# Kernel tuning notes

Measured on AMD Instinct MI355X. Metric: run time of the kernel, lower is better.

## Reference

```python
import jax, jax.numpy as jnp
import numpy as np

HIDDEN = 2048
NHEADS = 16
NKV = 4
HEAD_DIM = 128
B, T = 2, 2048


def setup_inputs() -> dict:
    key = jax.random.key(0)
    ks = jax.random.split(key, 7)
    x = jax.random.normal(ks[0], (B, T, HIDDEN), dtype=jnp.float32)
    # rope tables [T, head_dim//2]
    inv_freq = 1.0 / (10000.0 ** (jnp.arange(0, HEAD_DIM // 2, dtype=jnp.float32) / (HEAD_DIM // 2)))
    pos = jnp.arange(T, dtype=jnp.float32)
    ang = pos[:, None] * inv_freq[None, :]
    cos, sin = jnp.cos(ang), jnp.sin(ang)
    s = 0.02
    wq = jax.random.normal(ks[1], (HIDDEN, NHEADS * HEAD_DIM), dtype=jnp.float32) * s
    wk = jax.random.normal(ks[2], (HIDDEN, NKV * HEAD_DIM), dtype=jnp.float32) * s
    wv = jax.random.normal(ks[3], (HIDDEN, NKV * HEAD_DIM), dtype=jnp.float32) * s
    wo = jax.random.normal(ks[4], (NHEADS * HEAD_DIM, HIDDEN), dtype=jnp.float32) * s
    return {"x": x, "cos": cos, "sin": sin, "wq": wq, "wk": wk, "wv": wv, "wo": wo}


def _apply_rope(x, cos, sin):
    # x: [B, H, T, D]; cos/sin: [T, D//2]
    hd = x.shape[-1]
    x1, x2 = x[..., : hd // 2], x[..., hd // 2 :]
    c = cos[None, None, : x.shape[2], :]
    s = sin[None, None, : x.shape[2], :]
    return jnp.concatenate([x1 * c - x2 * s, x2 * c + x1 * s], axis=-1)


def reference(x, cos, sin, wq, wk, wv, wo):
    Bb, Tt, _ = x.shape
    q = (x @ wq).reshape(Bb, Tt, NHEADS, HEAD_DIM).transpose(0, 2, 1, 3)  # [B,H,T,D]
    k = (x @ wk).reshape(Bb, Tt, NKV, HEAD_DIM).transpose(0, 2, 1, 3)    # [B,Hk,T,D]
    v = (x @ wv).reshape(Bb, Tt, NKV, HEAD_DIM).transpose(0, 2, 1, 3)
    q = _apply_rope(q, cos, sin)
    k = _apply_rope(k, cos, sin)
    groups = NHEADS // NKV
    k = jnp.repeat(k, groups, axis=1)  # [B,H,T,D]
    v = jnp.repeat(v, groups, axis=1)
    scale = 1.0 / jnp.sqrt(jnp.asarray(HEAD_DIM, dtype=x.dtype))
    scores = jnp.einsum("bhqd,bhkd->bhqk", q, k) * scale
    causal = jnp.tril(jnp.ones((Tt, Tt), dtype=bool))
    scores = jnp.where(causal[None, None, :, :], scores, jnp.asarray(-jnp.inf, dtype=scores.dtype))
    attn = jax.nn.softmax(scores, axis=-1)
    out = jnp.einsum("bhqk,bhkd->bhqd", attn, v)
    out = out.transpose(0, 2, 1, 3).reshape(Bb, Tt, NHEADS * HEAD_DIM)
    return out @ wo
```

## Files before the change

### kernel.cpp

```cpp
#include <hip/hip_runtime.h>

#define HIDDEN 2048
#define NHEADS 16
#define NKV 4
#define HEAD_DIM 128
#define BB 2
#define TT 2048
#define MROWS (BB * TT)
#define NQKV (NHEADS * HEAD_DIM + 2 * NKV * HEAD_DIM)

typedef __attribute__((ext_vector_type(8))) short short8;
typedef __attribute__((ext_vector_type(4))) float f32x4;

#if __has_builtin(__builtin_amdgcn_exp2f)
#define EXP2F __builtin_amdgcn_exp2f
#else
#define EXP2F exp2f
#endif

__device__ __forceinline__ unsigned short f2bf(float f) {
    unsigned int u = __float_as_uint(f);
    unsigned int r = u + 0x7fffu + ((u >> 16) & 1u);
    return (unsigned short)(r >> 16);
}
__device__ __forceinline__ float b2f(unsigned short h) {
    return __uint_as_float(((unsigned int)h) << 16);
}

__device__ __forceinline__ void store_out(float* p, float v) { *p = v; }
__device__ __forceinline__ void store_out(unsigned short* p, float v) { *p = f2bf(v); }

__device__ __forceinline__ void load_lds_16(const void* g, void* l) {
    __builtin_amdgcn_global_load_lds((const __attribute__((address_space(1))) unsigned int*)g,
                                     (__attribute__((address_space(3))) unsigned int*)l,
                                     16, 0, 0);
}

__global__ void cast_x_kernel(const float* __restrict__ x, unsigned short* __restrict__ xb) {
    int i = blockIdx.x * 256 + threadIdx.x;
    float4 v = ((const float4*)x)[i];
    ushort4 o;
    o.x = f2bf(v.x); o.y = f2bf(v.y); o.z = f2bf(v.z); o.w = f2bf(v.w);
    ((ushort4*)xb)[i] = o;
}

__global__ void pack_wqkvT_kernel(const float* __restrict__ wq, const float* __restrict__ wk,
                                  const float* __restrict__ wv, unsigned short* __restrict__ out) {
    __shared__ float tile[32][33];
    int n0 = blockIdx.x * 32, k0 = blockIdx.y * 32;
    int tx = threadIdx.x, ty = threadIdx.y;
#pragma unroll
    for (int i = 0; i < 32; i += 8) {
        int k = k0 + ty + i;
        int n = n0 + tx;
        float v;
        if (n < 2048)      v = wq[(size_t)k * 2048 + n];
        else if (n < 2560) v = wk[(size_t)k * 512 + (n - 2048)];
        else               v = wv[(size_t)k * 512 + (n - 2560)];
        tile[ty + i][tx] = v;
    }
    __syncthreads();
#pragma unroll
    for (int i = 0; i < 32; i += 8) {
        int n = n0 + ty + i;
        int k = k0 + tx;
        out[(size_t)n * HIDDEN + k] = f2bf(tile[tx][ty + i]);
    }
}

__global__ void pack_woT_kernel(const float* __restrict__ wo, unsigned short* __restrict__ out) {
    __shared__ float tile[32][33];
    int n0 = blockIdx.x * 32, k0 = blockIdx.y * 32;
    int tx = threadIdx.x, ty = threadIdx.y;
#pragma unroll
    for (int i = 0; i < 32; i += 8)
        tile[ty + i][tx] = wo[(size_t)(k0 + ty + i) * HIDDEN + n0 + tx];
    __syncthreads();
#pragma unroll
    for (int i = 0; i < 32; i += 8)
        out[(size_t)(n0 + ty + i) * HIDDEN + k0 + tx] = f2bf(tile[tx][ty + i]);
}

template <typename OutT>
__global__ __launch_bounds__(256) void gemm_bt_kernel(const unsigned short* __restrict__ A,
                                                      const unsigned short* __restrict__ Bt,
                                                      OutT* __restrict__ C,
                                                      int M, int N, int K) {
    __shared__ __align__(16) unsigned short sA[128 * 32];
    __shared__ __align__(16) unsigned short sB[128 * 32];
    const int tid = threadIdx.x;
    const int lane = tid & 63, w = tid >> 6;
    const int quad = lane >> 4, l15 = lane & 15;
    const int wr = w >> 1, wc = w & 1;
    const int m0 = blockIdx.y * 128, n0 = blockIdx.x * 128;

    const unsigned short* gA = A + (size_t)(m0 + w * 16 + (lane >> 2)) * K + (lane & 3) * 8;
    const unsigned short* gB = Bt + (size_t)(n0 + w * 16 + (lane >> 2)) * K + (lane & 3) * 8;
    unsigned short* lA0 = &sA[(w * 16) * 32];
    unsigned short* lA1 = &sA[(64 + w * 16) * 32];
    unsigned short* lB0 = &sB[(w * 16) * 32];
    unsigned short* lB1 = &sB[(64 + w * 16) * 32];
    const size_t rstep = (size_t)64 * K;

    f32x4 acc[4][4];
    const f32x4 z4 = {0.f, 0.f, 0.f, 0.f};
#pragma unroll
    for (int mi = 0; mi < 4; ++mi)
#pragma unroll
        for (int ni = 0; ni < 4; ++ni) acc[mi][ni] = z4;

    for (int kk = 0; kk < K; kk += 32) {
        __syncthreads();
        load_lds_16(gA + kk, lA0);
        load_lds_16(gA + rstep + kk, lA1);
        load_lds_16(gB + kk, lB0);
        load_lds_16(gB + rstep + kk, lB1);
        __syncthreads();
        short8 af[4], bf[4];
#pragma unroll
        for (int i = 0; i < 4; ++i) {
            af[i] = *(const short8*)(&sA[(wr * 64 + i * 16 + l15) * 32 + quad * 8]);
            bf[i] = *(const short8*)(&sB[(wc * 64 + i * 16 + l15) * 32 + quad * 8]);
        }
#pragma unroll
        for (int mi = 0; mi < 4; ++mi)
#pragma unroll
            for (int ni = 0; ni < 4; ++ni)
                acc[mi][ni] = __builtin_amdgcn_mfma_f32_16x16x32_bf16(af[mi], bf[ni], acc[mi][ni], 0, 0, 0);
    }
#pragma unroll
    for (int mi = 0; mi < 4; ++mi)
#pragma unroll
        for (int ni = 0; ni < 4; ++ni)
#pragma unroll
            for (int r = 0; r < 4; ++r) {
                int gr = m0 + wr * 64 + mi * 16 + quad * 4 + r;
                int gc = n0 + wc * 64 + ni * 16 + l15;
                store_out(&C[(size_t)gr * N + gc], acc[mi][ni][r]);
            }
}

#define QP (MROWS * NHEADS * 64)
#define KP (MROWS * NKV * 64)
#define QSCL (0.08838834764831845f * 1.4426950408889634f)
__global__ void rope_kernel(const unsigned short* __restrict__ qkv,
                            const float* __restrict__ cosb, const float* __restrict__ sinb,
                            unsigned short* __restrict__ Q, unsigned short* __restrict__ K) {
    int tid = blockIdx.x * 256 + threadIdx.x;
    if (tid < QP) {
        int d = tid & 63;
        int h = (tid >> 6) & 15;
        int row = tid >> 10;
        int t = row & (TT - 1), b = row >> 11;
        float x1 = b2f(qkv[(size_t)row * NQKV + h * 128 + d]);
        float x2 = b2f(qkv[(size_t)row * NQKV + h * 128 + d + 64]);
        float c = cosb[t * 64 + d], s = sinb[t * 64 + d];
        unsigned short* dst = Q + ((size_t)(b * NHEADS + h) * TT + t) * 128 + d;
        dst[0]  = f2bf((x1 * c - x2 * s) * QSCL);
        dst[64] = f2bf((x2 * c + x1 * s) * QSCL);
    } else {
        int p = tid - QP;
        int d = p & 63;
        int kh = (p >> 6) & 3;
        int row = p >> 8;
        int t = row & (TT - 1), b = row >> 11;
        float x1 = b2f(qkv[(size_t)row * NQKV + 2048 + kh * 128 + d]);
        float x2 = b2f(qkv[(size_t)row * NQKV + 2048 + kh * 128 + d + 64]);
        float c = cosb[t * 64 + d], s = sinb[t * 64 + d];
        unsigned short* dst = K + ((size_t)(b * NKV + kh) * TT + t) * 128 + d;
        dst[0]  = f2bf(x1 * c - x2 * s);
        dst[64] = f2bf(x2 * c + x1 * s);
    }
}

__global__ void vtrans_kernel(const unsigned short* __restrict__ qkv,
                              unsigned short* __restrict__ Vt) {
    __shared__ unsigned short tile[32][33];
    int t0 = blockIdx.x * 32, d0 = blockIdx.y * 32, bz = blockIdx.z;
    int b = bz >> 2, kh = bz & 3;
    int tx = threadIdx.x, ty = threadIdx.y;
#pragma unroll
    for (int i = 0; i < 32; i += 8)
        tile[ty + i][tx] = qkv[(size_t)(b * TT + t0 + ty + i) * NQKV + 2560 + kh * 128 + d0 + tx];
    __syncthreads();
#pragma unroll
    for (int i = 0; i < 32; i += 8)
        Vt[((size_t)bz * 128 + d0 + ty + i) * TT + t0 + tx] = tile[tx][ty + i];
}

#define PS 68
__global__ __launch_bounds__(256) void flash_kernel(const unsigned short* __restrict__ Qb,
                                                    const unsigned short* __restrict__ Kb,
                                                    const unsigned short* __restrict__ Vtb,
                                                    unsigned short* __restrict__ Ob) {
    __shared__ __align__(16) unsigned short sK[4][64 * 32];
    __shared__ __align__(16) unsigned short sV[2][128 * 32];
    __shared__ __align__(16) unsigned short sP[4][32 * PS];

    const int tid = threadIdx.x;
    const int w = tid >> 6, lane = tid & 63;
    const int quad = lane >> 4, l15 = lane & 15;

    const int lin = blockIdx.x;
    const int e = lin >> 8;
    const int rem = lin & 255;
    const int h = rem & 15;
    const int b = (rem >> 4) & 1;
    const int j = rem >> 5;
    const int qb = e ? j : (15 - j);
    const int q0 = qb * 128;
    const int kvh = h >> 2;
    const unsigned short* Qh = Qb + (size_t)(b * NHEADS + h) * TT * 128;
    const unsigned short* Kh = Kb + (size_t)(b * NKV + kvh) * TT * 128;
    const unsigned short* Vth = Vtb + (size_t)(b * NKV + kvh) * 128 * TT;

    const int wrow0 = q0 + w * 32;

    const unsigned short* gK = Kh + (size_t)(lane >> 2) * 128 + w * 32 + (lane & 3) * 8;
    const int vkf = w >> 1;
    const unsigned short* gV = Vth + (size_t)((w & 1) * 64 + (lane >> 2)) * TT + vkf * 32 + (lane & 3) * 8;

    short8 aq[2][4];
#pragma unroll
    for (int mi = 0; mi < 2; ++mi)
#pragma unroll
        for (int dk = 0; dk < 4; ++dk)
            aq[mi][dk] = *(const short8*)(Qh + (size_t)(wrow0 + mi * 16 + l15) * 128 + dk * 32 + quad * 8);

    f32x4 accO[2][8], accL[2];
    const f32x4 z4 = {0.f, 0.f, 0.f, 0.f};
#pragma unroll
    for (int mi = 0; mi < 2; ++mi) {
        accL[mi] = z4;
#pragma unroll
        for (int nb = 0; nb < 8; ++nb) accO[mi][nb] = z4;
    }

    const short kone = (short)0x3F80;
    const short8 ones = {kone, kone, kone, kone, kone, kone, kone, kone};
    unsigned short* sPw = &sP[w][0];

    for (int kv0 = 0; kv0 < q0 + 128; kv0 += 64) {
        __syncthreads();
#pragma unroll
        for (int g = 0; g < 4; ++g)
            load_lds_16(gK + (size_t)(kv0 + g * 16) * 128, &sK[w][g * 512]);
#pragma unroll
        for (int jj = 0; jj < 4; ++jj)
            load_lds_16(gV + kv0 + (size_t)(jj * 16) * TT, &sV[vkf][((w & 1) * 64 + jj * 16) * 32]);
        __syncthreads();

        if (kv0 <= wrow0 + 31) {
            f32x4 sacc[2][4];
#pragma unroll
            for (int mi = 0; mi < 2; ++mi)
#pragma unroll
                for (int nh = 0; nh < 4; ++nh) sacc[mi][nh] = z4;
#pragma unroll
            for (int nh = 0; nh < 4; ++nh) {
#pragma unroll
                for (int dk = 0; dk < 4; ++dk) {
                    short8 bk = *(const short8*)(&sK[dk][(nh * 16 + l15) * 32 + quad * 8]);
                    sacc[0][nh] = __builtin_amdgcn_mfma_f32_16x16x32_bf16(aq[0][dk], bk, sacc[0][nh], 0, 0, 0);
                    sacc[1][nh] = __builtin_amdgcn_mfma_f32_16x16x32_bf16(aq[1][dk], bk, sacc[1][nh], 0, 0, 0);
                }
            }
#pragma unroll
            for (int mi = 0; mi < 2; ++mi) {
                const int fr0 = wrow0 + mi * 16;
                const bool needmask = (kv0 + 63) > fr0;
#pragma unroll
                for (int r = 0; r < 4; ++r) {
                    int row = fr0 + quad * 4 + r;
#pragma unroll
                    for (int nh = 0; nh < 4; ++nh) {
                        float s = sacc[mi][nh][r];
                        if (needmask) {
                            int col = kv0 + nh * 16 + l15;
                            s = (col <= row) ? s : -1e30f;
                        }
                        sPw[(mi * 16 + quad * 4 + r) * PS + nh * 16 + l15] = f2bf(EXP2F(s));
                    }
                }
            }
            __asm__ volatile("s_waitcnt lgkmcnt(0)" ::: "memory");
            short8 ap[2][2];
#pragma unroll
            for (int mi = 0; mi < 2; ++mi) {
#pragma unroll
                for (int kf = 0; kf < 2; ++kf)
                    ap[mi][kf] = *(const short8*)(&sPw[(mi * 16 + l15) * PS + kf * 32 + quad * 8]);
                accL[mi] = __builtin_amdgcn_mfma_f32_16x16x32_bf16(ap[mi][0], ones, accL[mi], 0, 0, 0);
                accL[mi] = __builtin_amdgcn_mfma_f32_16x16x32_bf16(ap[mi][1], ones, accL[mi], 0, 0, 0);
            }
#pragma unroll
            for (int nb = 0; nb < 8; ++nb) {
                short8 bv0 = *(const short8*)(&sV[0][(nb * 16 + l15) * 32 + quad * 8]);
                short8 bv1 = *(const short8*)(&sV[1][(nb * 16 + l15) * 32 + quad * 8]);
#pragma unroll
                for (int mi = 0; mi < 2; ++mi) {
                    accO[mi][nb] = __builtin_amdgcn_mfma_f32_16x16x32_bf16(ap[mi][0], bv0, accO[mi][nb], 0, 0, 0);
                    accO[mi][nb] = __builtin_amdgcn_mfma_f32_16x16x32_bf16(ap[mi][1], bv1, accO[mi][nb], 0, 0, 0);
                }
            }
        }
    }

    float inv[2][4];
#pragma unroll
    for (int mi = 0; mi < 2; ++mi)
#pragma unroll
        for (int r = 0; r < 4; ++r) inv[mi][r] = 1.0f / accL[mi][r];

    const size_t obase = ((size_t)b * TT + wrow0) * (NHEADS * HEAD_DIM) + h * 128;
#pragma unroll
    for (int half = 0; half < 2; ++half) {
        __asm__ volatile("s_waitcnt lgkmcnt(0)" ::: "memory");
#pragma unroll
        for (int mi = 0; mi < 2; ++mi)
#pragma unroll
            for (int nb2 = 0; nb2 < 4; ++nb2)
#pragma unroll
                for (int r = 0; r < 4; ++r)
                    sPw[(mi * 16 + quad * 4 + r) * PS + nb2 * 16 + l15] =
                        f2bf(accO[mi][half * 4 + nb2][r] * inv[mi][r]);
        __asm__ volatile("s_waitcnt lgkmcnt(0)" ::: "memory");
#pragma unroll
        for (int pass = 0; pass < 4; ++pass) {
            int row2 = pass * 8 + (lane >> 3);
            short8 vv = *(const short8*)(&sPw[row2 * PS + (lane & 7) * 8]);
            *(short8*)(Ob + obase + (size_t)row2 * (NHEADS * HEAD_DIM) + half * 64 + (lane & 7) * 8) = vv;
        }
    }
}

extern "C" void kernel_launch(void* const* d_in, const int* in_sizes, int n_in,
                              void* d_out, int out_size, void* d_ws, size_t ws_size,
                              hipStream_t stream) {
    const float* x    = (const float*)d_in[0];
    const float* cosb = (const float*)d_in[1];
    const float* sinb = (const float*)d_in[2];
    const float* wq   = (const float*)d_in[3];
    const float* wk   = (const float*)d_in[4];
    const float* wv   = (const float*)d_in[5];
    const float* wo   = (const float*)d_in[6];
    float* out = (float*)d_out;

    char* ws = (char*)d_ws;
    unsigned short* xb    = (unsigned short*)(ws);
    unsigned short* wqkvT = (unsigned short*)(ws + (16u << 20));
    unsigned short* woT   = (unsigned short*)(ws + (28u << 20));
    unsigned short* qkv   = (unsigned short*)(ws + (36u << 20));
    unsigned short* Qbuf  = (unsigned short*)(ws + (60u << 20));
    unsigned short* Kbuf  = (unsigned short*)(ws + (76u << 20));
    unsigned short* Vt    = (unsigned short*)(ws + (80u << 20));
    unsigned short* attn  = (unsigned short*)(ws + (84u << 20));

    cast_x_kernel<<<(MROWS * HIDDEN) / 4 / 256, 256, 0, stream>>>(x, xb);
    pack_wqkvT_kernel<<<dim3(NQKV / 32, HIDDEN / 32), dim3(32, 8), 0, stream>>>(wq, wk, wv, wqkvT);
    pack_woT_kernel<<<dim3(HIDDEN / 32, HIDDEN / 32), dim3(32, 8), 0, stream>>>(wo, woT);

    gemm_bt_kernel<unsigned short><<<dim3(NQKV / 128, MROWS / 128), 256, 0, stream>>>(
        xb, wqkvT, qkv, MROWS, NQKV, HIDDEN);

    rope_kernel<<<(QP + KP) / 256, 256, 0, stream>>>(qkv, cosb, sinb, Qbuf, Kbuf);
    vtrans_kernel<<<dim3(TT / 32, HEAD_DIM / 32, BB * NKV), dim3(32, 8), 0, stream>>>(qkv, Vt);

    flash_kernel<<<dim3(512), 256, 0, stream>>>(Qbuf, Kbuf, Vt, attn);

    gemm_bt_kernel<float><<<dim3(HIDDEN / 128, MROWS / 128), 256, 0, stream>>>(
        attn, woT, out, MROWS, HIDDEN, HIDDEN);
}
```

Before: 350.1 us.

## Split long causal query blocks across two KV halves and merge partial outputs

The 8 longest query blocks per head are now split into two work items covering the lower and upper halves of the KV range. Each writes unnormalized bf16 partial outputs and row sums to workspace, and a new merge kernel adds and normalizes them. The grid grows from 512 to 768 blocks to balance causal work across CUs. The QK^T MFMA operands are also swapped so each lane packs four P values into one 8-byte LDS store, and launch bounds now request 3 blocks per CU. The split costs an extra kernel launch, extra global traffic for the partials, and some precision loss from storing partials in bf16.

```diff
diff --git a/kernel.cpp b/kernel.cpp
--- a/kernel.cpp
+++ b/kernel.cpp
@@ -189,10 +189,12 @@
 }
 
 #define PS 68
-__global__ __launch_bounds__(256) void flash_kernel(const unsigned short* __restrict__ Qb,
-                                                    const unsigned short* __restrict__ Kb,
-                                                    const unsigned short* __restrict__ Vtb,
-                                                    unsigned short* __restrict__ Ob) {
+__global__ __launch_bounds__(256, 3) void flash_kernel(const unsigned short* __restrict__ Qb,
+                                                       const unsigned short* __restrict__ Kb,
+                                                       const unsigned short* __restrict__ Vtb,
+                                                       unsigned short* __restrict__ Ob,
+                                                       unsigned short* __restrict__ Po,
+                                                       float* __restrict__ Pl) {
     __shared__ __align__(16) unsigned short sK[4][64 * 32];
     __shared__ __align__(16) unsigned short sV[2][128 * 32];
     __shared__ __align__(16) unsigned short sP[4][32 * PS];
@@ -202,12 +204,22 @@
     const int quad = lane >> 4, l15 = lane & 15;
 
     const int lin = blockIdx.x;
-    const int e = lin >> 8;
+    const int member = lin >> 8;
     const int rem = lin & 255;
     const int h = rem & 15;
     const int b = (rem >> 4) & 1;
     const int j = rem >> 5;
-    const int qb = e ? j : (15 - j);
+    int qb, kvlo, kvhi;
+    bool partial;
+    if (member == 2) {
+        qb = j; kvlo = 0; kvhi = (qb + 1) * 128; partial = false;
+    } else {
+        qb = 15 - j;
+        int half = (qb + 1) * 64;
+        kvlo = member ? half : 0;
+        kvhi = member ? (qb + 1) * 128 : half;
+        partial = true;
+    }
     const int q0 = qb * 128;
     const int kvh = h >> 2;
     const unsigned short* Qh = Qb + (size_t)(b * NHEADS + h) * TT * 128;
@@ -240,7 +252,7 @@
     const short8 ones = {kone, kone, kone, kone, kone, kone, kone, kone};
     unsigned short* sPw = &sP[w][0];
 
-    for (int kv0 = 0; kv0 < q0 + 128; kv0 += 64) {
+    for (int kv0 = kvlo; kv0 < kvhi; kv0 += 64) {
         __syncthreads();
 #pragma unroll
         for (int g = 0; g < 4; ++g)
@@ -251,36 +263,36 @@
         __syncthreads();
 
         if (kv0 <= wrow0 + 31) {
-            f32x4 sacc[2][4];
-#pragma unroll
-            for (int mi = 0; mi < 2; ++mi)
-#pragma unroll
-                for (int nh = 0; nh < 4; ++nh) sacc[mi][nh] = z4;
-#pragma unroll
-            for (int nh = 0; nh < 4; ++nh) {
+            f32x4 st[4][2];
+#pragma unroll
+            for (int t = 0; t < 4; ++t)
+#pragma unroll
+                for (int h2 = 0; h2 < 2; ++h2) st[t][h2] = z4;
+#pragma unroll
+            for (int t = 0; t < 4; ++t) {
 #pragma unroll
                 for (int dk = 0; dk < 4; ++dk) {
-                    short8 bk = *(const short8*)(&sK[dk][(nh * 16 + l15) * 32 + quad * 8]);
-                    sacc[0][nh] = __builtin_amdgcn_mfma_f32_16x16x32_bf16(aq[0][dk], bk, sacc[0][nh], 0, 0, 0);
-                    sacc[1][nh] = __builtin_amdgcn_mfma_f32_16x16x32_bf16(aq[1][dk], bk, sacc[1][nh], 0, 0, 0);
+                    short8 ak = *(const short8*)(&sK[dk][(t * 16 + l15) * 32 + quad * 8]);
+                    st[t][0] = __builtin_amdgcn_mfma_f32_16x16x32_bf16(ak, aq[0][dk], st[t][0], 0, 0, 0);
+                    st[t][1] = __builtin_amdgcn_mfma_f32_16x16x32_bf16(ak, aq[1][dk], st[t][1], 0, 0, 0);
                 }
             }
 #pragma unroll
-            for (int mi = 0; mi < 2; ++mi) {
-                const int fr0 = wrow0 + mi * 16;
-                const bool needmask = (kv0 + 63) > fr0;
-#pragma unroll
-                for (int r = 0; r < 4; ++r) {
-                    int row = fr0 + quad * 4 + r;
-#pragma unroll
-                    for (int nh = 0; nh < 4; ++nh) {
-                        float s = sacc[mi][nh][r];
-                        if (needmask) {
-                            int col = kv0 + nh * 16 + l15;
-                            s = (col <= row) ? s : -1e30f;
-                        }
-                        sPw[(mi * 16 + quad * 4 + r) * PS + nh * 16 + l15] = f2bf(EXP2F(s));
+            for (int h2 = 0; h2 < 2; ++h2) {
+                const int rowbase = (h2 * 16 + l15) * PS;
+                const int qg = wrow0 + h2 * 16 + l15;
+#pragma unroll
+                for (int t = 0; t < 4; ++t) {
+                    const int kvb = kv0 + t * 16 + quad * 4;
+                    const bool nm = (kv0 + t * 16 + 15) > (wrow0 + h2 * 16);
+                    union { unsigned short u[4]; uint2 v; } pk;
+#pragma unroll
+                    for (int r = 0; r < 4; ++r) {
+                        float p = EXP2F(st[t][h2][r]);
+                        if (nm) p = (kvb + r <= qg) ? p : 0.f;
+                        pk.u[r] = f2bf(p);
                     }
+                    *(uint2*)(&sPw[rowbase + t * 16 + quad * 4]) = pk.v;
                 }
             }
             __asm__ volatile("s_waitcnt lgkmcnt(0)" ::: "memory");
@@ -306,32 +318,85 @@
         }
     }
 
-    float inv[2][4];
-#pragma unroll
-    for (int mi = 0; mi < 2; ++mi)
-#pragma unroll
-        for (int r = 0; r < 4; ++r) inv[mi][r] = 1.0f / accL[mi][r];
-
-    const size_t obase = ((size_t)b * TT + wrow0) * (NHEADS * HEAD_DIM) + h * 128;
-#pragma unroll
-    for (int half = 0; half < 2; ++half) {
-        __asm__ volatile("s_waitcnt lgkmcnt(0)" ::: "memory");
+    if (!partial) {
+        float inv[2][4];
 #pragma unroll
         for (int mi = 0; mi < 2; ++mi)
 #pragma unroll
-            for (int nb2 = 0; nb2 < 4; ++nb2)
+            for (int r = 0; r < 4; ++r) inv[mi][r] = 1.0f / accL[mi][r];
+
+        const size_t obase = ((size_t)b * TT + wrow0) * (NHEADS * HEAD_DIM) + h * 128;
+#pragma unroll
+        for (int half = 0; half < 2; ++half) {
+            __asm__ volatile("s_waitcnt lgkmcnt(0)" ::: "memory");
+#pragma unroll
+            for (int mi = 0; mi < 2; ++mi)
+#pragma unroll
+                for (int nb2 = 0; nb2 < 4; ++nb2)
+#pragma unroll
+                    for (int r = 0; r < 4; ++r)
+                        sPw[(mi * 16 + quad * 4 + r) * PS + nb2 * 16 + l15] =
+                            f2bf(accO[mi][half * 4 + nb2][r] * inv[mi][r]);
+            __asm__ volatile("s_waitcnt lgkmcnt(0)" ::: "memory");
+#pragma unroll
+            for (int pass = 0; pass < 4; ++pass) {
+                int row2 = pass * 8 + (lane >> 3);
+                short8 vv = *(const short8*)(&sPw[row2 * PS + (lane & 7) * 8]);
+                *(short8*)(Ob + obase + (size_t)row2 * (NHEADS * HEAD_DIM) + half * 64 + (lane & 7) * 8) = vv;
+            }
+        }
+    } else {
+        const int part = member;
+        const size_t pbase = ((size_t)(part * 2 + b) * 1024 + (wrow0 - 1024)) * 2048 + h * 128;
+#pragma unroll
+        for (int half = 0; half < 2; ++half) {
+            __asm__ volatile("s_waitcnt lgkmcnt(0)" ::: "memory");
+#pragma unroll
+            for (int mi = 0; mi < 2; ++mi)
+#pragma unroll
+                for (int nb2 = 0; nb2 < 4; ++nb2)
+#pragma unroll
+                    for (int r = 0; r < 4; ++r)
+                        sPw[(mi * 16 + quad * 4 + r) * PS + nb2 * 16 + l15] =
+                            f2bf(accO[mi][half * 4 + nb2][r]);
+            __asm__ volatile("s_waitcnt lgkmcnt(0)" ::: "memory");
+#pragma unroll
+            for (int pass = 0; pass < 4; ++pass) {
+                int row2 = pass * 8 + (lane >> 3);
+                short8 vv = *(const short8*)(&sPw[row2 * PS + (lane & 7) * 8]);
+                *(short8*)(Po + pbase + (size_t)row2 * 2048 + half * 64 + (lane & 7) * 8) = vv;
+            }
+        }
+        float* plb = Pl + ((size_t)(part * 2 + b) * 16 + h) * 1024 + (wrow0 - 1024);
+        if (l15 == 0) {
+#pragma unroll
+            for (int mi = 0; mi < 2; ++mi)
 #pragma unroll
                 for (int r = 0; r < 4; ++r)
-                    sPw[(mi * 16 + quad * 4 + r) * PS + nb2 * 16 + l15] =
-                        f2bf(accO[mi][half * 4 + nb2][r] * inv[mi][r]);
-        __asm__ volatile("s_waitcnt lgkmcnt(0)" ::: "memory");
-#pragma unroll
-        for (int pass = 0; pass < 4; ++pass) {
-            int row2 = pass * 8 + (lane >> 3);
-            short8 vv = *(const short8*)(&sPw[row2 * PS + (lane & 7) * 8]);
-            *(short8*)(Ob + obase + (size_t)row2 * (NHEADS * HEAD_DIM) + half * 64 + (lane & 7) * 8) = vv;
+                    plb[mi * 16 + quad * 4 + r] = accL[mi][r];
         }
     }
+}
+
+__global__ void merge_kernel(const unsigned short* __restrict__ Po, const float* __restrict__ Pl,
+                             unsigned short* __restrict__ attn) {
+    int gid = blockIdx.x * 256 + threadIdx.x;
+    size_t e8 = (size_t)gid * 8;
+    int col = (int)(e8 & 2047);
+    int rl  = (int)((e8 >> 11) & 1023);
+    int b   = (int)(e8 >> 21);
+    int h   = col >> 7;
+    size_t i0 = ((size_t)b * 1024 + rl) * 2048 + col;
+    size_t i1 = ((size_t)(2 + b) * 1024 + rl) * 2048 + col;
+    float l = Pl[((size_t)b * 16 + h) * 1024 + rl] + Pl[((size_t)(2 + b) * 16 + h) * 1024 + rl];
+    float inv = 1.0f / l;
+    union { uint4 v; unsigned short u[8]; } a, c, o;
+    a.v = *(const uint4*)(Po + i0);
+    c.v = *(const uint4*)(Po + i1);
+#pragma unroll
+    for (int k = 0; k < 8; ++k)
+        o.u[k] = f2bf((b2f(a.u[k]) + b2f(c.u[k])) * inv);
+    *(uint4*)(attn + ((size_t)b * 2048 + 1024 + rl) * 2048 + col) = o.v;
 }
 
 extern "C" void kernel_launch(void* const* d_in, const int* in_sizes, int n_in,
@@ -355,6 +420,8 @@
     unsigned short* Kbuf  = (unsigned short*)(ws + (76u << 20));
     unsigned short* Vt    = (unsigned short*)(ws + (80u << 20));
     unsigned short* attn  = (unsigned short*)(ws + (84u << 20));
+    unsigned short* Po    = (unsigned short*)(ws);
+    float*          Pl    = (float*)(ws + (16u << 20));
 
     cast_x_kernel<<<(MROWS * HIDDEN) / 4 / 256, 256, 0, stream>>>(x, xb);
     pack_wqkvT_kernel<<<dim3(NQKV / 32, HIDDEN / 32), dim3(32, 8), 0, stream>>>(wq, wk, wv, wqkvT);
@@ -366,7 +433,8 @@
     rope_kernel<<<(QP + KP) / 256, 256, 0, stream>>>(qkv, cosb, sinb, Qbuf, Kbuf);
     vtrans_kernel<<<dim3(TT / 32, HEAD_DIM / 32, BB * NKV), dim3(32, 8), 0, stream>>>(qkv, Vt);
 
-    flash_kernel<<<dim3(512), 256, 0, stream>>>(Qbuf, Kbuf, Vt, attn);
+    flash_kernel<<<dim3(768), 256, 0, stream>>>(Qbuf, Kbuf, Vt, attn, Po, Pl);
+    merge_kernel<<<dim3(2048), 256, 0, stream>>>(Po, Pl, attn);
 
     gemm_bt_kernel<float><<<dim3(HIDDEN / 128, MROWS / 128), 256, 0, stream>>>(
         attn, woT, out, MROWS, HIDDEN, HIDDEN);
```

New measurement: 334.1 us. 4.6% less time.
